# Performance work log

Hardware: AMD Instinct MI355X
Metric: run time of the kernel (lower is better)

Reference implementation:

```python
import jax, jax.numpy as jnp
import numpy as np

BT, N, D, HEADS, E = 1024, 64, 256, 4, 512
LRELU_SLOPE = 0.2
EPS = 1e-8


def setup_inputs() -> dict:
    key = jax.random.key(0)
    ks = jax.random.split(key, 8)
    d = D
    return {
        "H": jax.random.normal(ks[0], (BT, N, d), jnp.float32),
        "W_lin": jax.random.normal(ks[1], (d, d), jnp.float32) / np.sqrt(d).astype(np.float32),
        "W_val": jax.random.normal(ks[2], (d, d), jnp.float32) / np.sqrt(d).astype(np.float32),
        "a": jax.random.normal(ks[3], (HEADS, d // HEADS), jnp.float32),
        "W_out": jax.random.normal(ks[4], (d, d), jnp.float32) / np.sqrt(d).astype(np.float32),
        "A0": jax.random.uniform(ks[5], (N, N), jnp.float32),
        "src": jax.random.randint(ks[6], (E,), 0, N, jnp.int32),
        "dst": jax.random.randint(ks[7], (E,), 0, N, jnp.int32),
    }


def reference(H, W_lin, W_val, a, W_out, A0, src, dst):
    bt, n, d = H.shape
    h, dh = a.shape
    # projections (torch Linear: x @ W.T)
    Xq = (H @ W_lin.T).reshape(bt, n, h, dh)   # [BT,N,h,dh]
    Xv = (H @ W_val.T).reshape(bt, n, h, dh)
    # per-edge GATv2 scores: edge e goes dst[e] -> src[e] (src aggregates)
    Qs = Xq[:, src]                            # [BT,E,h,dh] receiving node
    Kt = Xq[:, dst]                            # [BT,E,h,dh] neighbor
    e = jnp.einsum('behd,hd->beh', jax.nn.leaky_relu(Qs + Kt, LRELU_SLOPE), a)
    e = e + jnp.log(A0[src, dst] + EPS)[None, :, None]   # anatomical bias
    # segment softmax over edges sharing the same receiving node (src)
    e_t = e.transpose(1, 0, 2)                 # [E,BT,h]
    m = jax.ops.segment_max(e_t, src, num_segments=n)    # [N,BT,h]
    ex = jnp.exp(e_t - m[src])
    denom = jax.ops.segment_sum(ex, src, num_segments=n)
    attn = ex / denom[src]                     # [E,BT,h]
    # weighted scatter of neighbor values
    Vt = Xv[:, dst].transpose(1, 0, 2, 3)      # [E,BT,h,dh]
    Y = jax.ops.segment_sum(attn[..., None] * Vt, src, num_segments=n)  # [N,BT,h,dh]
    Y = Y.transpose(1, 0, 2, 3).reshape(bt, n, d)
    return Y @ W_out.T
```

## Files before the change

### kernel.cpp

```cpp
#include <hip/hip_runtime.h>
#include <math.h>

#define D_    256
#define NE    512
#define NNODE 64
#define NHEAD 4
#define SLOPE 0.2f
#define BTN   65536

typedef __attribute__((ext_vector_type(4))) float f32x4;
typedef __attribute__((ext_vector_type(8))) _Float16 f16x8;
typedef __attribute__((ext_vector_type(2))) _Float16 f16x2;
typedef __attribute__((ext_vector_type(2))) __fp16   h16x2;
typedef unsigned short u16;

__device__ inline u16 f2h(float x) {
    union { _Float16 h; u16 u; } v; v.h = (_Float16)x; return v.u;
}
__device__ inline f16x2 pkrtz(float lo, float hi) {
    h16x2 r = __builtin_amdgcn_cvt_pkrtz(lo, hi);
    f16x2 o; __builtin_memcpy(&o, &r, 4); return o;
}

#define GLD16(g, l) __builtin_amdgcn_global_load_lds( \
    (const __attribute__((address_space(1))) void*)(g), \
    (__attribute__((address_space(3))) void*)(l), 16, 0, 0)

__global__ __launch_bounds__(512) void build_edge(const int* __restrict__ src,
    const int* __restrict__ dst, const float* __restrict__ A0,
    int2* __restrict__ gedge)
{
    const int t = threadIdx.x;
    int s = src[t], d = dst[t];
    float lg = logf(A0[s * NNODE + d] + 1e-8f);
    gedge[t] = make_int2((s << 8) | d, __float_as_int(lg));
}

__global__ __launch_bounds__(256) void prep_w3(const float* __restrict__ w0,
    const float* __restrict__ w1, const float* __restrict__ w2,
    u16* __restrict__ h0, u16* __restrict__ h1, u16* __restrict__ h2)
{
    int sel = blockIdx.x >> 6, b = blockIdx.x & 63;
    const float* s = sel == 0 ? w0 : sel == 1 ? w1 : w2;
    u16* h = sel == 0 ? h0 : sel == 1 ? h1 : h2;
    int i = b * 256 + threadIdx.x;
    float4 v = ((const float4*)s)[i];
    ((ushort4*)h)[i] = make_ushort4(f2h(v.x), f2h(v.y), f2h(v.z), f2h(v.w));
}

__global__ __launch_bounds__(256) void gemm12(const float* __restrict__ A32,
    const u16* __restrict__ B, u16* __restrict__ Xqh, u16* __restrict__ Xvt)
{
    __shared__ u16 sA[128 * 40];
    __shared__ u16 sB[4096];
    __shared__ u16 sT[16384];
    const int t = threadIdx.x, lane = t & 63, wave = t >> 6;
    const int wm = wave >> 1, wn = wave & 1;
    const int bid = blockIdx.x;
    const int swz = (bid & 7) * 256 + (bid >> 3);
    const int m0 = (swz >> 2) * 128, nq = swz & 3, n0 = nq * 128;
    const int fr = lane & 15, kq = (lane >> 4) * 8;

    f32x4 acc[4][4];
    #pragma unroll
    for (int i = 0; i < 4; ++i)
        #pragma unroll
        for (int j = 0; j < 4; ++j) acc[i][j] = 0.f;

    for (int k0 = 0; k0 < D_; k0 += 32) {
        #pragma unroll
        for (int rr = 0; rr < 2; ++rr) {
            int idx = rr * 256 + t;
            int row = idx >> 2, c8 = (idx & 3) * 8;
            const float* ap = A32 + (size_t)(m0 + row) * D_ + k0 + c8;
            float4 v0 = *(const float4*)ap;
            float4 v1 = *(const float4*)(ap + 4);
            f16x8 hv;
            hv[0] = (_Float16)v0.x; hv[1] = (_Float16)v0.y;
            hv[2] = (_Float16)v0.z; hv[3] = (_Float16)v0.w;
            hv[4] = (_Float16)v1.x; hv[5] = (_Float16)v1.y;
            hv[6] = (_Float16)v1.z; hv[7] = (_Float16)v1.w;
            *(f16x8*)&sA[row * 40 + c8] = hv;
        }
        #pragma unroll
        for (int s = 0; s < 2; ++s) {
            const int cb = (s * 4 + wave) * 64;
            const int c  = cb + lane;
            const int row = c >> 2, ks = (c & 3) * 8;
            GLD16(B + (size_t)(n0 + row) * D_ + k0 + ks, sB + cb * 8);
        }
        __syncthreads();

        f16x8 fa[4];
        #pragma unroll
        for (int mi = 0; mi < 4; ++mi)
            fa[mi] = *(const f16x8*)(sA + (wm * 64 + mi * 16 + fr) * 40 + kq);
        #pragma unroll
        for (int ni = 0; ni < 4; ++ni) {
            f16x8 fb = *(const f16x8*)(sB + (wn * 64 + ni * 16 + fr) * 32 + kq);
            #pragma unroll
            for (int mi = 0; mi < 4; ++mi)
                acc[mi][ni] = __builtin_amdgcn_mfma_f32_16x16x32_f16(fa[mi], fb, acc[mi][ni], 0, 0, 0);
        }
        __syncthreads();
    }

    const int fq = (lane >> 4) * 4;
    u16* wT = sT + wave * 4096;
    const bool isQ = nq < 2;
    #pragma unroll
    for (int mi = 0; mi < 4; ++mi)
        #pragma unroll
        for (int ni = 0; ni < 4; ++ni) {
            int node0 = mi * 16 + fq;
            int dim   = ni * 16 + fr;
            if (!isQ) {
                ushort4 v = make_ushort4(f2h(acc[mi][ni][0]), f2h(acc[mi][ni][1]),
                                         f2h(acc[mi][ni][2]), f2h(acc[mi][ni][3]));
                *(ushort4*)&wT[dim * 64 + (((node0 >> 3) ^ (dim & 7)) << 3) + (node0 & 7)] = v;
            } else {
                #pragma unroll
                for (int r = 0; r < 4; ++r) {
                    int node = node0 + r;
                    wT[node * 64 + ((((dim >> 3) ^ (node & 7))) << 3) + (dim & 7)]
                        = f2h(acc[mi][ni][r]);
                }
            }
        }
    __syncthreads();
    const int btq = (m0 >> 6) + wm;
    const int hq  = isQ ? (n0 >> 6) + wn : ((n0 - 256) >> 6) + wn;
    u16* gx = (isQ ? Xqh : Xvt) + ((size_t)btq * NHEAD + hq) * 4096;
    #pragma unroll
    for (int r = 0; r < 8; ++r)
        *(f16x8*)&gx[r * 512 + lane * 8] = *(const f16x8*)&wT[r * 512 + lane * 8];
}

__global__ __launch_bounds__(256) void gemm3(const u16* __restrict__ A,
    const u16* __restrict__ B, float* __restrict__ Cout)
{
    __shared__ u16 sA[4096], sB[4096];
    const int t = threadIdx.x, lane = t & 63, wave = t >> 6;
    const int wm = wave >> 1, wn = wave & 1;
    const int bid = blockIdx.x;
    const int swz = (bid & 7) * 128 + (bid >> 3);
    const int m0 = (swz >> 1) * 128, n0 = (swz & 1) * 128;
    const int fr = lane & 15, kq = (lane >> 4) * 8;

    f32x4 acc[4][4];
    #pragma unroll
    for (int i = 0; i < 4; ++i)
        #pragma unroll
        for (int j = 0; j < 4; ++j) acc[i][j] = 0.f;

    for (int k0 = 0; k0 < D_; k0 += 32) {
        #pragma unroll
        for (int s = 0; s < 2; ++s) {
            const int cb = (s * 4 + wave) * 64;
            const int c  = cb + lane;
            const int row = c >> 2, ks = (c & 3) * 8;
            GLD16(A + (size_t)(m0 + row) * D_ + k0 + ks, sA + cb * 8);
            GLD16(B + (size_t)(n0 + row) * D_ + k0 + ks, sB + cb * 8);
        }
        __syncthreads();

        f16x8 fa[4];
        #pragma unroll
        for (int mi = 0; mi < 4; ++mi)
            fa[mi] = *(const f16x8*)(sA + (wm * 64 + mi * 16 + fr) * 32 + kq);
        #pragma unroll
        for (int ni = 0; ni < 4; ++ni) {
            f16x8 fb = *(const f16x8*)(sB + (wn * 64 + ni * 16 + fr) * 32 + kq);
            #pragma unroll
            for (int mi = 0; mi < 4; ++mi)
                acc[mi][ni] = __builtin_amdgcn_mfma_f32_16x16x32_f16(fa[mi], fb, acc[mi][ni], 0, 0, 0);
        }
        __syncthreads();
    }

    const int fq = (lane >> 4) * 4;
    #pragma unroll
    for (int mi = 0; mi < 4; ++mi)
        #pragma unroll
        for (int ni = 0; ni < 4; ++ni)
            #pragma unroll
            for (int r = 0; r < 4; ++r) {
                int m = m0 + wm * 64 + mi * 16 + fq + r;
                int n = n0 + wn * 64 + ni * 16 + fr;
                Cout[(size_t)m * D_ + n] = acc[mi][ni][r];
            }
}

__global__ __launch_bounds__(256, 5) void fused_edge_agg(
    const u16* __restrict__ Xqh, const u16* __restrict__ Xvt,
    const int2* __restrict__ gedge, const float* __restrict__ a,
    u16* __restrict__ Yh)
{
    __shared__ u16   sQ[4096];
    __shared__ float sP[4096];
    __shared__ float sBn[NNODE];
    __shared__ float sLin[NE];
    __shared__ int   sPack[NE];

    const int t = threadIdx.x, lane = t & 63, wave = t >> 6;
    const int fr = lane & 15, qtr = lane >> 4;
    const int bt = blockIdx.x >> 2, h = blockIdx.x & 3;

    const u16* gv = Xvt + ((size_t)bt * NHEAD + h) * 4096;
    f16x8 vf[2][4];
    #pragma unroll
    for (int kk = 0; kk < 2; ++kk) {
        int g = kk * 4 + qtr;
        #pragma unroll
        for (int mi = 0; mi < 4; ++mi) {
            int arow = mi * 16 + fr;
            vf[kk][mi] = *(const f16x8*)&gv[arow * 64 + ((g ^ (arow & 7)) << 3)];
        }
    }
    f16x8 af[2];
    #pragma unroll
    for (int kk = 0; kk < 2; ++kk) {
        const float* ab = a + h * 64 + kk * 32 + qtr * 8;
        float4 a0 = *(const float4*)ab, a1 = *(const float4*)(ab + 4);
        af[kk][0] = (_Float16)(0.4f * a0.x); af[kk][1] = (_Float16)(0.4f * a0.y);
        af[kk][2] = (_Float16)(0.4f * a0.z); af[kk][3] = (_Float16)(0.4f * a0.w);
        af[kk][4] = (_Float16)(0.4f * a1.x); af[kk][5] = (_Float16)(0.4f * a1.y);
        af[kk][6] = (_Float16)(0.4f * a1.z); af[kk][7] = (_Float16)(0.4f * a1.w);
    }

    const u16* gq = Xqh + ((size_t)bt * NHEAD + h) * 4096;
    #pragma unroll
    for (int r = 0; r < 2; ++r) {
        int id = r * 256 + t;
        GLD16(gq + id * 8, (char*)sQ + id * 16);
    }
    #pragma unroll
    for (int i = 0; i < 4; ++i)
        ((float4*)sP)[t + i * 256] = make_float4(0.f, 0.f, 0.f, 0.f);
    __syncthreads();

    {
        int n = t >> 2, qq = t & 3;
        float b = 0.f;
        #pragma unroll
        for (int j = 0; j < 2; ++j) {
            int ck = qq * 2 + j;
            f16x8 qv = *(const f16x8*)&sQ[n * 64 + ((ck ^ (n & 7)) << 3)];
            const float* ab = a + h * 64 + ck * 8;
            float4 a0 = *(const float4*)ab, a1 = *(const float4*)(ab + 4);
            b = fmaf((float)qv[0], a0.x, b); b = fmaf((float)qv[1], a0.y, b);
            b = fmaf((float)qv[2], a0.z, b); b = fmaf((float)qv[3], a0.w, b);
            b = fmaf((float)qv[4], a1.x, b); b = fmaf((float)qv[5], a1.y, b);
            b = fmaf((float)qv[6], a1.z, b); b = fmaf((float)qv[7], a1.w, b);
        }
        b += __shfl_xor(b, 1);
        b += __shfl_xor(b, 2);
        if (qq == 0) sBn[n] = b;
    }
    __syncthreads();

    #pragma unroll
    for (int i = 0; i < 2; ++i) {
        int e = t + i * 256;
        int2 ge = gedge[e];
        int s_ = ge.x >> 8, d_ = ge.x & 255;
        sPack[e] = ge.x;
        sLin[e] = 0.6f * (sBn[s_] + sBn[d_]) + __int_as_float(ge.y);
    }
    __syncthreads();

    const int wbase = wave * 128;
    #pragma unroll
    for (int tt = 0; tt < 8; ++tt) {
        int e = wbase + tt * 16 + fr;
        int pk = sPack[e];
        int s_ = pk >> 8, d_ = pk & 255;
        f32x4 acc = 0.f;
        #pragma unroll
        for (int kk = 0; kk < 2; ++kk) {
            int ck = kk * 4 + qtr;
            f16x8 qs = *(const f16x8*)&sQ[s_ * 64 + ((ck ^ (s_ & 7)) << 3)];
            f16x8 qd = *(const f16x8*)&sQ[d_ * 64 + ((ck ^ (d_ & 7)) << 3)];
            f16x8 x = qs + qd;
            unsigned xu[4];
            __builtin_memcpy(xu, &x, 16);
            xu[0] &= 0x7FFF7FFFu; xu[1] &= 0x7FFF7FFFu;
            xu[2] &= 0x7FFF7FFFu; xu[3] &= 0x7FFF7FFFu;
            f16x8 xa;
            __builtin_memcpy(&xa, xu, 16);
            acc = __builtin_amdgcn_mfma_f32_16x16x32_f16(xa, af[kk], acc, 0, 0, 0);
        }
        int c = lane & 15;
        if (c < 4) {
            float av = c == 0 ? acc[0] : c == 1 ? acc[1] : c == 2 ? acc[2] : acc[3];
            int eg = wbase + tt * 16 + qtr * 4 + c;
            int pk2 = sPack[eg];
            atomicAdd(&sP[(pk2 >> 8) * 64 + (pk2 & 255)], __expf(av + sLin[eg]));
        }
    }
    __syncthreads();

    {
        int s_ = t >> 2, qq = t & 3;
        const float4* row = (const float4*)&sP[s_ * 64 + qq * 16];
        float4 v0 = row[0], v1 = row[1], v2 = row[2], v3 = row[3];
        float part = v0.x + v0.y + v0.z + v0.w + v1.x + v1.y + v1.z + v1.w
                   + v2.x + v2.y + v2.z + v2.w + v3.x + v3.y + v3.z + v3.w;
        part += __shfl_xor(part, 1);
        part += __shfl_xor(part, 2);
        float inv = part > 0.f ? 1.f / part : 0.f;
        f16x2 p0 = pkrtz(v0.x * inv, v0.y * inv), p1 = pkrtz(v0.z * inv, v0.w * inv);
        f16x2 p2 = pkrtz(v1.x * inv, v1.y * inv), p3 = pkrtz(v1.z * inv, v1.w * inv);
        f16x2 p4 = pkrtz(v2.x * inv, v2.y * inv), p5 = pkrtz(v2.z * inv, v2.w * inv);
        f16x2 p6 = pkrtz(v3.x * inv, v3.y * inv), p7 = pkrtz(v3.z * inv, v3.w * inv);
        int c0 = qq * 2, c1 = qq * 2 + 1;
        u16* d0 = &sQ[s_ * 64 + ((c0 ^ (s_ & 7)) << 3)];
        u16* d1 = &sQ[s_ * 64 + ((c1 ^ (s_ & 7)) << 3)];
        ((f16x2*)d0)[0] = p0; ((f16x2*)d0)[1] = p1;
        ((f16x2*)d0)[2] = p2; ((f16x2*)d0)[3] = p3;
        ((f16x2*)d1)[0] = p4; ((f16x2*)d1)[1] = p5;
        ((f16x2*)d1)[2] = p6; ((f16x2*)d1)[3] = p7;
    }
    __syncthreads();

    f32x4 acc[4];
    #pragma unroll
    for (int i = 0; i < 4; ++i) acc[i] = 0.f;
    const int srow = wave * 16 + fr;
    #pragma unroll
    for (int kk = 0; kk < 2; ++kk) {
        int g = kk * 4 + qtr;
        f16x8 fb = *(const f16x8*)&sQ[srow * 64 + ((g ^ (srow & 7)) << 3)];
        #pragma unroll
        for (int mi = 0; mi < 4; ++mi)
            acc[mi] = __builtin_amdgcn_mfma_f32_16x16x32_f16(vf[kk][mi], fb, acc[mi], 0, 0, 0);
    }

    const int node = wave * 16 + fr;
    const int fq = qtr * 4;
    u16* yh = Yh + ((size_t)bt * NNODE + node) * D_ + h * 64;
    #pragma unroll
    for (int mi = 0; mi < 4; ++mi) {
        ushort4 v = make_ushort4(f2h(acc[mi][0]), f2h(acc[mi][1]),
                                 f2h(acc[mi][2]), f2h(acc[mi][3]));
        *(ushort4*)&yh[mi * 16 + fq] = v;
    }
}

extern "C" void kernel_launch(void* const* d_in, const int* in_sizes, int n_in,
                              void* d_out, int out_size, void* d_ws, size_t ws_size,
                              hipStream_t stream)
{
    const float* H     = (const float*)d_in[0];
    const float* W_lin = (const float*)d_in[1];
    const float* W_val = (const float*)d_in[2];
    const float* a     = (const float*)d_in[3];
    const float* W_out = (const float*)d_in[4];
    const float* A0    = (const float*)d_in[5];
    const int*   src   = (const int*)d_in[6];
    const int*   dst   = (const int*)d_in[7];

    const size_t nX = (size_t)BTN * D_;
    u16*  Xqh   = (u16*)d_ws;
    u16*  Yh    = Xqh + nX;
    u16*  Wqv   = Yh + nX;
    u16*  Wouth = Wqv + 512 * D_;
    int2* gedge = (int2*)(Wouth + D_ * D_);
    if (ws_size < (size_t)134217728) return;

    u16* Xvt = (u16*)d_out;

    build_edge<<<1, 512, 0, stream>>>(src, dst, A0, gedge);
    prep_w3<<<192, 256, 0, stream>>>(W_lin, W_val, W_out,
                                     Wqv, Wqv + D_ * D_, Wouth);

    gemm12<<<2048, 256, 0, stream>>>(H, Wqv, Xqh, Xvt);

    fused_edge_agg<<<4096, 256, 0, stream>>>(Xqh, Xvt, gedge, a, Yh);

    gemm3<<<1024, 256, 0, stream>>>(Yh, Wouth, (float*)d_out);
}
```

Before: 104.5 us.

## Register-prefetch next A tile and alias LDS buffers in gemm12

Loads the next k-slice of the fp32 A input into registers before the barrier and MFMA work, so global load latency overlaps compute instead of stalling at the start of each iteration. The separate sA/sB/sT shared arrays are merged into one aliased buffer, since the transpose scratch is only used after the main loop. This lowers LDS per block, which may allow more resident blocks. The cost is more live registers for the prefetch buffers.

```diff
diff --git a/kernel.cpp b/kernel.cpp
--- a/kernel.cpp
+++ b/kernel.cpp
@@ -51,15 +51,16 @@
 __global__ __launch_bounds__(256) void gemm12(const float* __restrict__ A32,
     const u16* __restrict__ B, u16* __restrict__ Xqh, u16* __restrict__ Xvt)
 {
-    __shared__ u16 sA[128 * 40];
-    __shared__ u16 sB[4096];
-    __shared__ u16 sT[16384];
+    __shared__ u16 smem[16384];
+    u16* sA = smem;
+    u16* sB = smem + 5120;
     const int t = threadIdx.x, lane = t & 63, wave = t >> 6;
     const int wm = wave >> 1, wn = wave & 1;
     const int bid = blockIdx.x;
     const int swz = (bid & 7) * 256 + (bid >> 3);
     const int m0 = (swz >> 2) * 128, nq = swz & 3, n0 = nq * 128;
     const int fr = lane & 15, kq = (lane >> 4) * 8;
+    const int arow_ = t >> 2, ac8 = (t & 3) * 8;
 
     f32x4 acc[4][4];
     #pragma unroll
@@ -67,20 +68,23 @@
         #pragma unroll
         for (int j = 0; j < 4; ++j) acc[i][j] = 0.f;
 
+    float4 pv0[2], pv1[2];
+    #pragma unroll
+    for (int rr = 0; rr < 2; ++rr) {
+        const float* ap = A32 + (size_t)(m0 + rr * 64 + arow_) * D_ + ac8;
+        pv0[rr] = *(const float4*)ap;
+        pv1[rr] = *(const float4*)(ap + 4);
+    }
+
     for (int k0 = 0; k0 < D_; k0 += 32) {
         #pragma unroll
         for (int rr = 0; rr < 2; ++rr) {
-            int idx = rr * 256 + t;
-            int row = idx >> 2, c8 = (idx & 3) * 8;
-            const float* ap = A32 + (size_t)(m0 + row) * D_ + k0 + c8;
-            float4 v0 = *(const float4*)ap;
-            float4 v1 = *(const float4*)(ap + 4);
             f16x8 hv;
-            hv[0] = (_Float16)v0.x; hv[1] = (_Float16)v0.y;
-            hv[2] = (_Float16)v0.z; hv[3] = (_Float16)v0.w;
-            hv[4] = (_Float16)v1.x; hv[5] = (_Float16)v1.y;
-            hv[6] = (_Float16)v1.z; hv[7] = (_Float16)v1.w;
-            *(f16x8*)&sA[row * 40 + c8] = hv;
+            hv[0] = (_Float16)pv0[rr].x; hv[1] = (_Float16)pv0[rr].y;
+            hv[2] = (_Float16)pv0[rr].z; hv[3] = (_Float16)pv0[rr].w;
+            hv[4] = (_Float16)pv1[rr].x; hv[5] = (_Float16)pv1[rr].y;
+            hv[6] = (_Float16)pv1[rr].z; hv[7] = (_Float16)pv1[rr].w;
+            *(f16x8*)&sA[(rr * 64 + arow_) * 40 + ac8] = hv;
         }
         #pragma unroll
         for (int s = 0; s < 2; ++s) {
@@ -89,6 +93,15 @@
             const int row = c >> 2, ks = (c & 3) * 8;
             GLD16(B + (size_t)(n0 + row) * D_ + k0 + ks, sB + cb * 8);
         }
+        if (k0 + 32 < D_) {
+            #pragma unroll
+            for (int rr = 0; rr < 2; ++rr) {
+                const float* ap = A32 + (size_t)(m0 + rr * 64 + arow_) * D_
+                                + k0 + 32 + ac8;
+                pv0[rr] = *(const float4*)ap;
+                pv1[rr] = *(const float4*)(ap + 4);
+            }
+        }
         __syncthreads();
 
         f16x8 fa[4];
@@ -106,7 +119,7 @@
     }
 
     const int fq = (lane >> 4) * 4;
-    u16* wT = sT + wave * 4096;
+    u16* wT = smem + wave * 4096;
     const bool isQ = nq < 2;
     #pragma unroll
     for (int mi = 0; mi < 4; ++mi)
```

Measured after the change: 104.8 us. No clear change (+0.3%).

## Load GEMM fragments directly from global memory into registers, dropping LDS staging

Applied to the files above, without the earlier changes.

The projection GEMM no longer stages A and B tiles through shared memory with two barriers per k-step. Each wave now loads its own MFMA fragments straight from global memory, converting fp32 A to fp16 with packed round-toward-zero conversion. Shared memory shrinks to the epilogue transpose buffer, and launch bounds ask for 4 blocks per SM. In exchange, both waves sharing a row or column load the same data redundantly, so it is now reused only through cache. Rounding mode for A also changes from round-to-nearest to truncation.

```diff
diff --git a/kernel.cpp b/kernel.cpp
--- a/kernel.cpp
+++ b/kernel.cpp
@@ -21,6 +21,16 @@
     h16x2 r = __builtin_amdgcn_cvt_pkrtz(lo, hi);
     f16x2 o; __builtin_memcpy(&o, &r, 4); return o;
 }
+__device__ inline f16x8 pack8(float4 v0, float4 v1) {
+    f16x2 a = pkrtz(v0.x, v0.y), b = pkrtz(v0.z, v0.w);
+    f16x2 c = pkrtz(v1.x, v1.y), d = pkrtz(v1.z, v1.w);
+    f16x8 o;
+    __builtin_memcpy(&o, &a, 4);
+    __builtin_memcpy((char*)&o + 4, &b, 4);
+    __builtin_memcpy((char*)&o + 8, &c, 4);
+    __builtin_memcpy((char*)&o + 12, &d, 4);
+    return o;
+}
 
 #define GLD16(g, l) __builtin_amdgcn_global_load_lds( \
     (const __attribute__((address_space(1))) void*)(g), \
@@ -48,12 +58,10 @@
     ((ushort4*)h)[i] = make_ushort4(f2h(v.x), f2h(v.y), f2h(v.z), f2h(v.w));
 }
 
-__global__ __launch_bounds__(256) void gemm12(const float* __restrict__ A32,
+__global__ __launch_bounds__(256, 4) void gemm12(const float* __restrict__ A32,
     const u16* __restrict__ B, u16* __restrict__ Xqh, u16* __restrict__ Xvt)
 {
-    __shared__ u16 sA[128 * 40];
-    __shared__ u16 sB[4096];
-    __shared__ u16 sT[16384];
+    __shared__ u16 smem[16384];
     const int t = threadIdx.x, lane = t & 63, wave = t >> 6;
     const int wm = wave >> 1, wn = wave & 1;
     const int bid = blockIdx.x;
@@ -67,46 +75,29 @@
         #pragma unroll
         for (int j = 0; j < 4; ++j) acc[i][j] = 0.f;
 
+    const float* aBase = A32 + (size_t)(m0 + wm * 64 + fr) * D_ + kq;
+    const u16*   bBase = B   + (size_t)(n0 + wn * 64 + fr) * D_ + kq;
+
     for (int k0 = 0; k0 < D_; k0 += 32) {
-        #pragma unroll
-        for (int rr = 0; rr < 2; ++rr) {
-            int idx = rr * 256 + t;
-            int row = idx >> 2, c8 = (idx & 3) * 8;
-            const float* ap = A32 + (size_t)(m0 + row) * D_ + k0 + c8;
+        f16x8 fa[4];
+        #pragma unroll
+        for (int mi = 0; mi < 4; ++mi) {
+            const float* ap = aBase + (size_t)(mi * 16) * D_ + k0;
             float4 v0 = *(const float4*)ap;
             float4 v1 = *(const float4*)(ap + 4);
-            f16x8 hv;
-            hv[0] = (_Float16)v0.x; hv[1] = (_Float16)v0.y;
-            hv[2] = (_Float16)v0.z; hv[3] = (_Float16)v0.w;
-            hv[4] = (_Float16)v1.x; hv[5] = (_Float16)v1.y;
-            hv[6] = (_Float16)v1.z; hv[7] = (_Float16)v1.w;
-            *(f16x8*)&sA[row * 40 + c8] = hv;
-        }
-        #pragma unroll
-        for (int s = 0; s < 2; ++s) {
-            const int cb = (s * 4 + wave) * 64;
-            const int c  = cb + lane;
-            const int row = c >> 2, ks = (c & 3) * 8;
-            GLD16(B + (size_t)(n0 + row) * D_ + k0 + ks, sB + cb * 8);
-        }
-        __syncthreads();
-
-        f16x8 fa[4];
-        #pragma unroll
-        for (int mi = 0; mi < 4; ++mi)
-            fa[mi] = *(const f16x8*)(sA + (wm * 64 + mi * 16 + fr) * 40 + kq);
+            fa[mi] = pack8(v0, v1);
+        }
         #pragma unroll
         for (int ni = 0; ni < 4; ++ni) {
-            f16x8 fb = *(const f16x8*)(sB + (wn * 64 + ni * 16 + fr) * 32 + kq);
+            f16x8 fb = *(const f16x8*)(bBase + (size_t)(ni * 16) * D_ + k0);
             #pragma unroll
             for (int mi = 0; mi < 4; ++mi)
                 acc[mi][ni] = __builtin_amdgcn_mfma_f32_16x16x32_f16(fa[mi], fb, acc[mi][ni], 0, 0, 0);
         }
-        __syncthreads();
     }
 
     const int fq = (lane >> 4) * 4;
-    u16* wT = sT + wave * 4096;
+    u16* wT = smem + wave * 4096;
     const bool isQ = nq < 2;
     #pragma unroll
     for (int mi = 0; mi < 4; ++mi)
```

After: 167.6 us. 60.4% more time.

## Pre-convert H to fp16 and load GEMM A tiles asynchronously into LDS

Applied to the files above, without the earlier changes.

Adds a separate pass that converts H from fp32 to fp16 into workspace, so the projection GEMM can stream A tiles with direct global-to-LDS loads instead of converting in registers. The GEMM epilogue reuses the A/B tile LDS for the transpose staging in two passes, cutting shared memory per block. The edge kernel drops its per-edge LDS tables and recomputes the bias from global edge data, raising the occupancy hint from 5 to 6. The cost is an extra full read and write of H through an additional kernel launch.

```diff
diff --git a/kernel.cpp b/kernel.cpp
--- a/kernel.cpp
+++ b/kernel.cpp
@@ -36,6 +36,15 @@
     gedge[t] = make_int2((s << 8) | d, __float_as_int(lg));
 }
 
+__global__ __launch_bounds__(256) void prep_hi(const float* __restrict__ s,
+    u16* __restrict__ h, int n4)
+{
+    for (int i = blockIdx.x * 256 + threadIdx.x; i < n4; i += gridDim.x * 256) {
+        float4 v = ((const float4*)s)[i];
+        ((ushort4*)h)[i] = make_ushort4(f2h(v.x), f2h(v.y), f2h(v.z), f2h(v.w));
+    }
+}
+
 __global__ __launch_bounds__(256) void prep_w3(const float* __restrict__ w0,
     const float* __restrict__ w1, const float* __restrict__ w2,
     u16* __restrict__ h0, u16* __restrict__ h1, u16* __restrict__ h2)
@@ -48,12 +57,12 @@
     ((ushort4*)h)[i] = make_ushort4(f2h(v.x), f2h(v.y), f2h(v.z), f2h(v.w));
 }
 
-__global__ __launch_bounds__(256) void gemm12(const float* __restrict__ A32,
+__global__ __launch_bounds__(256) void gemm12f(const u16* __restrict__ A,
     const u16* __restrict__ B, u16* __restrict__ Xqh, u16* __restrict__ Xvt)
 {
-    __shared__ u16 sA[128 * 40];
-    __shared__ u16 sB[4096];
-    __shared__ u16 sT[16384];
+    __shared__ u16 smem[8192];
+    u16* sA = smem;
+    u16* sB = smem + 4096;
     const int t = threadIdx.x, lane = t & 63, wave = t >> 6;
     const int wm = wave >> 1, wn = wave & 1;
     const int bid = blockIdx.x;
@@ -69,24 +78,11 @@
 
     for (int k0 = 0; k0 < D_; k0 += 32) {
         #pragma unroll
-        for (int rr = 0; rr < 2; ++rr) {
-            int idx = rr * 256 + t;
-            int row = idx >> 2, c8 = (idx & 3) * 8;
-            const float* ap = A32 + (size_t)(m0 + row) * D_ + k0 + c8;
-            float4 v0 = *(const float4*)ap;
-            float4 v1 = *(const float4*)(ap + 4);
-            f16x8 hv;
-            hv[0] = (_Float16)v0.x; hv[1] = (_Float16)v0.y;
-            hv[2] = (_Float16)v0.z; hv[3] = (_Float16)v0.w;
-            hv[4] = (_Float16)v1.x; hv[5] = (_Float16)v1.y;
-            hv[6] = (_Float16)v1.z; hv[7] = (_Float16)v1.w;
-            *(f16x8*)&sA[row * 40 + c8] = hv;
-        }
-        #pragma unroll
         for (int s = 0; s < 2; ++s) {
             const int cb = (s * 4 + wave) * 64;
             const int c  = cb + lane;
             const int row = c >> 2, ks = (c & 3) * 8;
+            GLD16(A + (size_t)(m0 + row) * D_ + k0 + ks, sA + cb * 8);
             GLD16(B + (size_t)(n0 + row) * D_ + k0 + ks, sB + cb * 8);
         }
         __syncthreads();
@@ -94,7 +90,7 @@
         f16x8 fa[4];
         #pragma unroll
         for (int mi = 0; mi < 4; ++mi)
-            fa[mi] = *(const f16x8*)(sA + (wm * 64 + mi * 16 + fr) * 40 + kq);
+            fa[mi] = *(const f16x8*)(sA + (wm * 64 + mi * 16 + fr) * 32 + kq);
         #pragma unroll
         for (int ni = 0; ni < 4; ++ni) {
             f16x8 fb = *(const f16x8*)(sB + (wn * 64 + ni * 16 + fr) * 32 + kq);
@@ -106,34 +102,39 @@
     }
 
     const int fq = (lane >> 4) * 4;
-    u16* wT = sT + wave * 4096;
     const bool isQ = nq < 2;
-    #pragma unroll
-    for (int mi = 0; mi < 4; ++mi)
-        #pragma unroll
-        for (int ni = 0; ni < 4; ++ni) {
-            int node0 = mi * 16 + fq;
-            int dim   = ni * 16 + fr;
-            if (!isQ) {
-                ushort4 v = make_ushort4(f2h(acc[mi][ni][0]), f2h(acc[mi][ni][1]),
-                                         f2h(acc[mi][ni][2]), f2h(acc[mi][ni][3]));
-                *(ushort4*)&wT[dim * 64 + (((node0 >> 3) ^ (dim & 7)) << 3) + (node0 & 7)] = v;
-            } else {
-                #pragma unroll
-                for (int r = 0; r < 4; ++r) {
-                    int node = node0 + r;
-                    wT[node * 64 + ((((dim >> 3) ^ (node & 7))) << 3) + (dim & 7)]
-                        = f2h(acc[mi][ni][r]);
-                }
-            }
-        }
-    __syncthreads();
     const int btq = (m0 >> 6) + wm;
     const int hq  = isQ ? (n0 >> 6) + wn : ((n0 - 256) >> 6) + wn;
     u16* gx = (isQ ? Xqh : Xvt) + ((size_t)btq * NHEAD + hq) * 4096;
-    #pragma unroll
-    for (int r = 0; r < 8; ++r)
-        *(f16x8*)&gx[r * 512 + lane * 8] = *(const f16x8*)&wT[r * 512 + lane * 8];
+    u16* wT = smem + wn * 4096;
+    #pragma unroll
+    for (int pass = 0; pass < 2; ++pass) {
+        if (wm == pass) {
+            #pragma unroll
+            for (int mi = 0; mi < 4; ++mi)
+                #pragma unroll
+                for (int ni = 0; ni < 4; ++ni) {
+                    int node0 = mi * 16 + fq;
+                    int dim   = ni * 16 + fr;
+                    if (!isQ) {
+                        ushort4 v = make_ushort4(f2h(acc[mi][ni][0]), f2h(acc[mi][ni][1]),
+                                                 f2h(acc[mi][ni][2]), f2h(acc[mi][ni][3]));
+                        *(ushort4*)&wT[dim * 64 + (((node0 >> 3) ^ (dim & 7)) << 3) + (node0 & 7)] = v;
+                    } else {
+                        #pragma unroll
+                        for (int r = 0; r < 4; ++r) {
+                            int node = node0 + r;
+                            wT[node * 64 + ((((dim >> 3) ^ (node & 7))) << 3) + (dim & 7)]
+                                = f2h(acc[mi][ni][r]);
+                        }
+                    }
+                }
+            #pragma unroll
+            for (int r = 0; r < 8; ++r)
+                *(f16x8*)&gx[r * 512 + lane * 8] = *(const f16x8*)&wT[r * 512 + lane * 8];
+        }
+        __syncthreads();
+    }
 }
 
 __global__ __launch_bounds__(256) void gemm3(const u16* __restrict__ A,
@@ -191,7 +192,7 @@
             }
 }
 
-__global__ __launch_bounds__(256, 5) void fused_edge_agg(
+__global__ __launch_bounds__(256, 6) void fused_edge_agg(
     const u16* __restrict__ Xqh, const u16* __restrict__ Xvt,
     const int2* __restrict__ gedge, const float* __restrict__ a,
     u16* __restrict__ Yh)
@@ -199,8 +200,6 @@
     __shared__ u16   sQ[4096];
     __shared__ float sP[4096];
     __shared__ float sBn[NNODE];
-    __shared__ float sLin[NE];
-    __shared__ int   sPack[NE];
 
     const int t = threadIdx.x, lane = t & 63, wave = t >> 6;
     const int fr = lane & 15, qtr = lane >> 4;
@@ -259,22 +258,12 @@
     }
     __syncthreads();
 
-    #pragma unroll
-    for (int i = 0; i < 2; ++i) {
-        int e = t + i * 256;
+    const int wbase = wave * 128;
+    #pragma unroll
+    for (int tt = 0; tt < 8; ++tt) {
+        int e = wbase + tt * 16 + fr;
         int2 ge = gedge[e];
         int s_ = ge.x >> 8, d_ = ge.x & 255;
-        sPack[e] = ge.x;
-        sLin[e] = 0.6f * (sBn[s_] + sBn[d_]) + __int_as_float(ge.y);
-    }
-    __syncthreads();
-
-    const int wbase = wave * 128;
-    #pragma unroll
-    for (int tt = 0; tt < 8; ++tt) {
-        int e = wbase + tt * 16 + fr;
-        int pk = sPack[e];
-        int s_ = pk >> 8, d_ = pk & 255;
         f32x4 acc = 0.f;
         #pragma unroll
         for (int kk = 0; kk < 2; ++kk) {
@@ -294,8 +283,10 @@
         if (c < 4) {
             float av = c == 0 ? acc[0] : c == 1 ? acc[1] : c == 2 ? acc[2] : acc[3];
             int eg = wbase + tt * 16 + qtr * 4 + c;
-            int pk2 = sPack[eg];
-            atomicAdd(&sP[(pk2 >> 8) * 64 + (pk2 & 255)], __expf(av + sLin[eg]));
+            int2 ge2 = gedge[eg];
+            int s2 = ge2.x >> 8, d2 = ge2.x & 255;
+            float lin = 0.6f * (sBn[s2] + sBn[d2]) + __int_as_float(ge2.y);
+            atomicAdd(&sP[s2 * 64 + d2], __expf(av + lin));
         }
     }
     __syncthreads();
@@ -361,11 +352,12 @@
     const int*   dst   = (const int*)d_in[7];
 
     const size_t nX = (size_t)BTN * D_;
-    u16*  Xqh   = (u16*)d_ws;
-    u16*  Yh    = Xqh + nX;
-    u16*  Wqv   = Yh + nX;
+    u16*  Hh    = (u16*)d_ws;
+    u16*  Xqh   = Hh + nX;
+    u16*  Wqv   = Xqh + nX;
     u16*  Wouth = Wqv + 512 * D_;
     int2* gedge = (int2*)(Wouth + D_ * D_);
+    u16*  Yh    = Hh;
     if (ws_size < (size_t)134217728) return;
 
     u16* Xvt = (u16*)d_out;
@@ -373,8 +365,9 @@
     build_edge<<<1, 512, 0, stream>>>(src, dst, A0, gedge);
     prep_w3<<<192, 256, 0, stream>>>(W_lin, W_val, W_out,
                                      Wqv, Wqv + D_ * D_, Wouth);
-
-    gemm12<<<2048, 256, 0, stream>>>(H, Wqv, Xqh, Xvt);
+    prep_hi<<<4096, 256, 0, stream>>>(H, Hh, (int)(nX / 4));
+
+    gemm12f<<<2048, 256, 0, stream>>>(Hh, Wqv, Xqh, Xvt);
 
     fused_edge_agg<<<4096, 256, 0, stream>>>(Xqh, Xvt, gedge, a, Yh);
 
```

New measurement: 126.3 us. 20.9% more time.
